# Optimization experiments

Measured on AMD Instinct MI355X. Metric: run time of the kernel, lower is better.

The kernel has to match this reference:

```python
import jax, jax.numpy as jnp
import numpy as np
import math

B, Q_LEN, D, H, KV = 8, 2048, 1024, 16, 256
HD = D // H

def setup_inputs() -> dict:
    key0 = jax.random.key(0)
    ks = jax.random.split(key0, 6)
    query = jax.random.normal(ks[0], (B, Q_LEN, D), dtype=jnp.float32)
    key = jax.random.normal(ks[1], (B, 1024), dtype=jnp.float32)
    value = jax.random.normal(ks[2], (B, 1024), dtype=jnp.float32)
    clip_score = jax.random.uniform(ks[3], (B, KV), dtype=jnp.float32)
    # k_linear / v_linear weights (embed_dim, 1024), no bias
    k_weight = jax.random.normal(ks[4], (D, 1024), dtype=jnp.float32) * 0.02
    v_weight = jax.random.normal(ks[5], (D, 1024), dtype=jnp.float32) * 0.02
    # scale_linear: Linear(512, 1), weight const 0.05, bias const 7.5 (per nn.init.constant_)
    scale_w = jnp.full((2 * KV,), 0.05, dtype=jnp.float32)
    scale_b = jnp.array(7.5, dtype=jnp.float32)
    return {"query": query, "key": key, "value": value, "clip_score": clip_score,
            "k_weight": k_weight, "v_weight": v_weight, "scale_w": scale_w, "scale_b": scale_b}

def reference(query, key, value, clip_score, k_weight, v_weight, scale_w, scale_b):
    act_scale = 1.0
    b, qlen, d = query.shape
    # key/value are (B,1024): expand to (B,KV,1024) as in torch branch
    key_e = jnp.broadcast_to(key[:, None, :], (b, KV, key.shape[-1]))
    val_e = jnp.broadcast_to(value[:, None, :], (b, KV, value.shape[-1]))
    K = jnp.einsum('bkc,dc->bkd', key_e, k_weight)   # (B,KV,D)
    V = jnp.einsum('bkc,dc->bkd', val_e, v_weight)   # (B,KV,D)
    Qh = query.reshape(b, qlen, H, HD).transpose(0, 2, 1, 3)  # (B,H,Q,HD)
    Kh = K.reshape(b, KV, H, HD).transpose(0, 2, 1, 3)        # (B,H,KV,HD)
    Vh = V.reshape(b, KV, H, HD).transpose(0, 2, 1, 3)        # (B,H,KV,HD)
    scores = jnp.einsum('bhqd,bhkd->bhqk', Qh, Kh) / math.sqrt(HD)  # (B,H,Q,KV)
    # scale_linear(cat([scores, clip], -1)) == scores@w1 + clip@w2 + b (avoid materializing concat)
    w1, w2 = scale_w[:KV], scale_w[KV:]
    lin = (jnp.einsum('bhqk,k->bhq', scores, w1)[..., None]
           + (clip_score @ w2)[:, None, None, None] + scale_b)   # (B,H,Q,1)
    clip_e = clip_score[:, None, None, :]                        # (B,1,1,KV)
    scores = scores + (lin * clip_e) * act_scale
    attn_weights = jax.nn.softmax(scores, axis=-1)
    out = jnp.einsum('bhqk,bhkd->bhqd', attn_weights, Vh)
    out = out.transpose(0, 2, 1, 3).reshape(b, qlen, d)
    return (out, attn_weights)
```

## Files before the change

### kernel.cpp

```cpp
#include <hip/hip_runtime.h>
#include <hip/hip_bf16.h>

#define B_    8
#define QLEN  2048
#define D_    1024
#define H_    16
#define KV_   256
#define HD_   64

typedef float fvec4 __attribute__((ext_vector_type(4)));

#define WS_KVEC 0
#define WS_VVEC 8192
#define WS_C2   16384
#define WS_SW1  16392
#define WS_L    16400

__device__ inline float wave_sum(float v) {
#pragma unroll
  for (int off = 32; off > 0; off >>= 1) v += __shfl_xor(v, off, 64);
  return v;
}
__device__ inline float wave_max(float v) {
#pragma unroll
  for (int off = 32; off > 0; off >>= 1) v = fmaxf(v, __shfl_xor(v, off, 64));
  return v;
}
__device__ inline float wave_min(float v) {
#pragma unroll
  for (int off = 32; off > 0; off >>= 1) v = fminf(v, __shfl_xor(v, off, 64));
  return v;
}
template <int N>
__device__ inline void multi_sum(float* v) {
#pragma unroll
  for (int off = 32; off > 0; off >>= 1) {
#pragma unroll
    for (int r = 0; r < N; ++r) v[r] += __shfl_xor(v[r], off, 64);
  }
}

__global__ __launch_bounds__(256) void prep_kernel(
    const float* __restrict__ key, const float* __restrict__ value,
    const float* __restrict__ kw, const float* __restrict__ vw,
    const float* __restrict__ clip, const float* __restrict__ scale_w,
    float* __restrict__ ws) {
  const int lane = threadIdx.x & 63;
  const int waveId = threadIdx.x >> 6;

  if (blockIdx.x == 1024) {
    if (waveId != 0) return;
    const float4* sw4 = reinterpret_cast<const float4*>(scale_w);
    float4 a = sw4[lane];
    float s = wave_sum(a.x + a.y + a.z + a.w);
    if (lane == 0) ws[WS_SW1] = s;
    float4 w2 = sw4[64 + lane];
    for (int b = 0; b < B_; ++b) {
      const float4* c4 = reinterpret_cast<const float4*>(clip + b * KV_);
      float4 c = c4[lane];
      float p = c.x * w2.x + c.y * w2.y + c.z * w2.z + c.w * w2.w;
      p = wave_sum(p);
      if (lane == 0) ws[WS_C2 + b] = p;
    }
    return;
  }

  const int W = blockIdx.x * 4 + waveId;
  const int sel = W >> 11;
  const int rem = W & 2047;
  const int b = rem >> 8;
  const int g = rem & 255;
  const float* x = (sel ? value : key) + b * 1024;
  const float* Wt = sel ? vw : kw;
  const float4* x4 = reinterpret_cast<const float4*>(x);
  float4 xs[4];
#pragma unroll
  for (int i = 0; i < 4; ++i) xs[i] = x4[i * 64 + lane];
  float* outv = ws + (sel ? WS_VVEC : WS_KVEC) + b * 1024;
  float acc[4];
#pragma unroll
  for (int r = 0; r < 4; ++r) {
    const int d = g * 4 + r;
    const float4* w4 = reinterpret_cast<const float4*>(Wt + (size_t)d * 1024);
    acc[r] = 0.f;
#pragma unroll
    for (int i = 0; i < 4; ++i) {
      float4 w = w4[i * 64 + lane];
      acc[r] += xs[i].x * w.x + xs[i].y * w.y + xs[i].z * w.z + xs[i].w * w.w;
    }
  }
  multi_sum<4>(acc);
  if (lane < 4) outv[g * 4 + lane] = acc[lane];
}

__global__ __launch_bounds__(256) void qdot_kernel(
    const float* __restrict__ query, const float* __restrict__ scale_b,
    float* __restrict__ ws) {
  const int lane = threadIdx.x & 63;
  const int waveId = threadIdx.x >> 6;
  const int rowBase = blockIdx.x * 64 + waveId * 16;
  const int b = rowBase >> 15;
  const int h = (rowBase >> 11) & 15;
  const int q0 = rowBase & 2047;
  const int g = lane >> 4;
  const int c = lane & 15;

  const fvec4 kvv = reinterpret_cast<const fvec4*>(ws + WS_KVEC + b * 1024 + h * HD_)[c];
  const float sw1 = ws[WS_SW1];
  const float Lc = ws[WS_C2 + b] + scale_b[0];

  const float* qb = query + ((size_t)(b * QLEN + q0)) * D_ + h * HD_;
  float p[4];
#pragma unroll
  for (int j = 0; j < 4; ++j) {
    const fvec4 q4 = __builtin_nontemporal_load(
        reinterpret_cast<const fvec4*>(qb + (size_t)(j * 4 + g) * D_) + c);
    p[j] = q4.x * kvv.x + q4.y * kvv.y + q4.z * kvv.z + q4.w * kvv.w;
  }
#pragma unroll
  for (int off = 1; off <= 8; off <<= 1) {
#pragma unroll
    for (int j = 0; j < 4; ++j) p[j] += __shfl_xor(p[j], off, 64);
  }
  if (c < 4) {
    const float sp = (c == 0) ? p[0] : (c == 1) ? p[1] : (c == 2) ? p[2] : p[3];
    ws[WS_L + rowBase + c * 4 + g] = sw1 * (sp * 0.125f) + Lc;
  }
}

__global__ __launch_bounds__(256) void stream_kernel(
    const float* __restrict__ clip, const float* __restrict__ ws,
    float* __restrict__ attn, float* __restrict__ out) {
  const int lane = threadIdx.x & 63;
  const int gwave = (blockIdx.x * 256 + threadIdx.x) >> 6;
  const int row0 = gwave * 32;
  const int b = row0 >> 15;

  const fvec4 cl = reinterpret_cast<const fvec4*>(clip + b * KV_)[lane];
  const float cmax = wave_max(fmaxf(fmaxf(cl.x, cl.y), fmaxf(cl.z, cl.w)));
  const float cmin = wave_min(fminf(fminf(cl.x, cl.y), fminf(cl.z, cl.w)));
  const float* Lp = ws + WS_L + row0;

  fvec4* a4 = reinterpret_cast<fvec4*>(attn) + (size_t)row0 * 64 + lane;
#pragma unroll 4
  for (int i = 0; i < 32; ++i) {
    const float Ld = Lp[i];
    const float m = (Ld >= 0.f) ? Ld * cmax : Ld * cmin;
    fvec4 e;
    e.x = __expf(Ld * cl.x - m);
    e.y = __expf(Ld * cl.y - m);
    e.z = __expf(Ld * cl.z - m);
    e.w = __expf(Ld * cl.w - m);
    const float den = wave_sum(e.x + e.y + e.z + e.w);
    e *= (1.0f / den);
    __builtin_nontemporal_store(e, &a4[(size_t)i * 64]);
  }

  const fvec4* v4 = reinterpret_cast<const fvec4*>(ws + WS_VVEC);
  fvec4* o4 = reinterpret_cast<fvec4*>(out);
#pragma unroll
  for (int i = 0; i < 8; ++i) {
    const int j = (gwave * 8 + i) * 64 + lane;
    const int ob = j >> 19;
    const int d4 = j & 255;
    fvec4 v = v4[ob * 256 + d4];
    __builtin_nontemporal_store(v, &o4[j]);
  }
}

extern "C" void kernel_launch(void* const* d_in, const int* in_sizes, int n_in,
                              void* d_out, int out_size, void* d_ws, size_t ws_size,
                              hipStream_t stream) {
  const float* query   = (const float*)d_in[0];
  const float* key     = (const float*)d_in[1];
  const float* value   = (const float*)d_in[2];
  const float* clip    = (const float*)d_in[3];
  const float* kw      = (const float*)d_in[4];
  const float* vw      = (const float*)d_in[5];
  const float* scale_w = (const float*)d_in[6];
  const float* scale_b = (const float*)d_in[7];
  float* out  = (float*)d_out;
  float* attn = out + (size_t)B_ * QLEN * D_;
  float* ws   = (float*)d_ws;

  hipLaunchKernelGGL(prep_kernel, dim3(1025), dim3(256), 0, stream,
                     key, value, kw, vw, clip, scale_w, ws);
  hipLaunchKernelGGL(qdot_kernel, dim3(4096), dim3(256), 0, stream,
                     query, scale_b, ws);
  hipLaunchKernelGGL(stream_kernel, dim3(2048), dim3(256), 0, stream,
                     clip, ws, attn, out);
}
```

Measured before the change: 82.93 us.

## Reuse weight rows across batches in prep and move out-broadcast into qdot kernel

The prep kernel now loads each weight row once into registers and loops over all 8 batches, so it launches 129 blocks instead of 1025 and stops re-reading the weight matrices 8 times. The broadcast write of V into the output tensor moves from the attention-stream kernel into extra blocks of the qdot kernel. This lets the output writes overlap with the query reads, and the stream kernel writes only attention weights. The stream kernel also fetches its 32 row coefficients in a single vector load and takes each one with readlane, with the loop fully unrolled.

```diff
diff --git a/kernel.cpp b/kernel.cpp
--- a/kernel.cpp
+++ b/kernel.cpp
@@ -48,16 +48,16 @@
   const int lane = threadIdx.x & 63;
   const int waveId = threadIdx.x >> 6;
 
-  if (blockIdx.x == 1024) {
+  if (blockIdx.x == 128) {
     if (waveId != 0) return;
-    const float4* sw4 = reinterpret_cast<const float4*>(scale_w);
-    float4 a = sw4[lane];
+    const fvec4* sw4 = reinterpret_cast<const fvec4*>(scale_w);
+    fvec4 a = sw4[lane];
     float s = wave_sum(a.x + a.y + a.z + a.w);
     if (lane == 0) ws[WS_SW1] = s;
-    float4 w2 = sw4[64 + lane];
+    fvec4 w2 = sw4[64 + lane];
     for (int b = 0; b < B_; ++b) {
-      const float4* c4 = reinterpret_cast<const float4*>(clip + b * KV_);
-      float4 c = c4[lane];
+      const fvec4* c4 = reinterpret_cast<const fvec4*>(clip + b * KV_);
+      fvec4 c = c4[lane];
       float p = c.x * w2.x + c.y * w2.y + c.z * w2.z + c.w * w2.w;
       p = wave_sum(p);
       if (lane == 0) ws[WS_C2 + b] = p;
@@ -66,39 +66,66 @@
   }
 
   const int W = blockIdx.x * 4 + waveId;
-  const int sel = W >> 11;
-  const int rem = W & 2047;
-  const int b = rem >> 8;
-  const int g = rem & 255;
-  const float* x = (sel ? value : key) + b * 1024;
+  const int sel = W >> 8;
+  const int g = W & 255;
   const float* Wt = sel ? vw : kw;
-  const float4* x4 = reinterpret_cast<const float4*>(x);
-  float4 xs[4];
-#pragma unroll
-  for (int i = 0; i < 4; ++i) xs[i] = x4[i * 64 + lane];
-  float* outv = ws + (sel ? WS_VVEC : WS_KVEC) + b * 1024;
-  float acc[4];
+  const float* xsrc = sel ? value : key;
+  float* outv = ws + (sel ? WS_VVEC : WS_KVEC);
+
+  fvec4 wr[4][4];
 #pragma unroll
   for (int r = 0; r < 4; ++r) {
-    const int d = g * 4 + r;
-    const float4* w4 = reinterpret_cast<const float4*>(Wt + (size_t)d * 1024);
-    acc[r] = 0.f;
-#pragma unroll
-    for (int i = 0; i < 4; ++i) {
-      float4 w = w4[i * 64 + lane];
-      acc[r] += xs[i].x * w.x + xs[i].y * w.y + xs[i].z * w.z + xs[i].w * w.w;
-    }
-  }
-  multi_sum<4>(acc);
-  if (lane < 4) outv[g * 4 + lane] = acc[lane];
-}
-
-__global__ __launch_bounds__(256) void qdot_kernel(
+    const fvec4* w4 = reinterpret_cast<const fvec4*>(Wt + (size_t)(g * 4 + r) * 1024);
+#pragma unroll
+    for (int i = 0; i < 4; ++i) wr[r][i] = w4[i * 64 + lane];
+  }
+
+  for (int b = 0; b < B_; ++b) {
+    const fvec4* x4 = reinterpret_cast<const fvec4*>(xsrc + b * 1024);
+    fvec4 xs[4];
+#pragma unroll
+    for (int i = 0; i < 4; ++i) xs[i] = x4[i * 64 + lane];
+    float acc[4];
+#pragma unroll
+    for (int r = 0; r < 4; ++r) {
+      acc[r] = 0.f;
+#pragma unroll
+      for (int i = 0; i < 4; ++i) {
+        acc[r] += xs[i].x * wr[r][i].x + xs[i].y * wr[r][i].y +
+                  xs[i].z * wr[r][i].z + xs[i].w * wr[r][i].w;
+      }
+    }
+    multi_sum<4>(acc);
+    if (lane < 4) {
+      const float v = (lane == 0) ? acc[0] : (lane == 1) ? acc[1]
+                    : (lane == 2) ? acc[2] : acc[3];
+      outv[b * 1024 + g * 4 + lane] = v;
+    }
+  }
+}
+
+__global__ __launch_bounds__(256) void qdot_out_kernel(
     const float* __restrict__ query, const float* __restrict__ scale_b,
-    float* __restrict__ ws) {
+    float* __restrict__ ws, float* __restrict__ out) {
   const int lane = threadIdx.x & 63;
+
+  if (blockIdx.x < 1024) {
+    const fvec4* v4 = reinterpret_cast<const fvec4*>(ws + WS_VVEC);
+    fvec4* o4 = reinterpret_cast<fvec4*>(out);
+    const int idx = blockIdx.x * 256 + threadIdx.x;
+#pragma unroll
+    for (int i = 0; i < 16; ++i) {
+      const int j = idx + i * 262144;
+      const int ob = j >> 19;
+      const int d4 = j & 255;
+      fvec4 v = v4[ob * 256 + d4];
+      __builtin_nontemporal_store(v, &o4[j]);
+    }
+    return;
+  }
+
   const int waveId = threadIdx.x >> 6;
-  const int rowBase = blockIdx.x * 64 + waveId * 16;
+  const int rowBase = (blockIdx.x - 1024) * 64 + waveId * 16;
   const int b = rowBase >> 15;
   const int h = (rowBase >> 11) & 15;
   const int q0 = rowBase & 2047;
@@ -128,9 +155,9 @@
   }
 }
 
-__global__ __launch_bounds__(256) void stream_kernel(
+__global__ __launch_bounds__(256) void attn_stream_kernel(
     const float* __restrict__ clip, const float* __restrict__ ws,
-    float* __restrict__ attn, float* __restrict__ out) {
+    float* __restrict__ attn) {
   const int lane = threadIdx.x & 63;
   const int gwave = (blockIdx.x * 256 + threadIdx.x) >> 6;
   const int row0 = gwave * 32;
@@ -139,12 +166,13 @@
   const fvec4 cl = reinterpret_cast<const fvec4*>(clip + b * KV_)[lane];
   const float cmax = wave_max(fmaxf(fmaxf(cl.x, cl.y), fmaxf(cl.z, cl.w)));
   const float cmin = wave_min(fminf(fminf(cl.x, cl.y), fminf(cl.z, cl.w)));
-  const float* Lp = ws + WS_L + row0;
+
+  const float Lv = ws[WS_L + row0 + (lane & 31)];
 
   fvec4* a4 = reinterpret_cast<fvec4*>(attn) + (size_t)row0 * 64 + lane;
-#pragma unroll 4
+#pragma unroll
   for (int i = 0; i < 32; ++i) {
-    const float Ld = Lp[i];
+    const float Ld = __builtin_amdgcn_readlane(Lv, i);
     const float m = (Ld >= 0.f) ? Ld * cmax : Ld * cmin;
     fvec4 e;
     e.x = __expf(Ld * cl.x - m);
@@ -154,17 +182,6 @@
     const float den = wave_sum(e.x + e.y + e.z + e.w);
     e *= (1.0f / den);
     __builtin_nontemporal_store(e, &a4[(size_t)i * 64]);
-  }
-
-  const fvec4* v4 = reinterpret_cast<const fvec4*>(ws + WS_VVEC);
-  fvec4* o4 = reinterpret_cast<fvec4*>(out);
-#pragma unroll
-  for (int i = 0; i < 8; ++i) {
-    const int j = (gwave * 8 + i) * 64 + lane;
-    const int ob = j >> 19;
-    const int d4 = j & 255;
-    fvec4 v = v4[ob * 256 + d4];
-    __builtin_nontemporal_store(v, &o4[j]);
   }
 }
 
@@ -183,10 +200,10 @@
   float* attn = out + (size_t)B_ * QLEN * D_;
   float* ws   = (float*)d_ws;
 
-  hipLaunchKernelGGL(prep_kernel, dim3(1025), dim3(256), 0, stream,
+  hipLaunchKernelGGL(prep_kernel, dim3(129), dim3(256), 0, stream,
                      key, value, kw, vw, clip, scale_w, ws);
-  hipLaunchKernelGGL(qdot_kernel, dim3(4096), dim3(256), 0, stream,
-                     query, scale_b, ws);
-  hipLaunchKernelGGL(stream_kernel, dim3(2048), dim3(256), 0, stream,
-                     clip, ws, attn, out);
-}
+  hipLaunchKernelGGL(qdot_out_kernel, dim3(5120), dim3(256), 0, stream,
+                     query, scale_b, ws, out);
+  hipLaunchKernelGGL(attn_stream_kernel, dim3(2048), dim3(256), 0, stream,
+                     clip, ws, attn);
+}
```

Measured after the change: 92.87 us. 1.12x slower.

## Fuse query-dot and softmax streaming kernels; load each weight row once in prep

Applied to the files above, without the earlier changes.

Merges the qdot and stream kernels into one. Each wave computes its 32 rows' scale logits in registers and broadcasts them with readlane, so the logit array no longer goes through the workspace and one launch is dropped. The prep kernel is restructured so each wave loads one weight row once and reuses it across all 8 batches, instead of rereading the weight matrix once per batch. This cuts weight traffic about eightfold and halves the prep grid, at the cost of more registers and fully unrolled loops in the fused kernel.

```diff
diff --git a/kernel.cpp b/kernel.cpp
--- a/kernel.cpp
+++ b/kernel.cpp
@@ -14,7 +14,6 @@
 #define WS_VVEC 8192
 #define WS_C2   16384
 #define WS_SW1  16392
-#define WS_L    16400
 
 __device__ inline float wave_sum(float v) {
 #pragma unroll
@@ -48,16 +47,16 @@
   const int lane = threadIdx.x & 63;
   const int waveId = threadIdx.x >> 6;
 
-  if (blockIdx.x == 1024) {
+  if (blockIdx.x == 512) {
     if (waveId != 0) return;
-    const float4* sw4 = reinterpret_cast<const float4*>(scale_w);
-    float4 a = sw4[lane];
+    const fvec4* sw4 = reinterpret_cast<const fvec4*>(scale_w);
+    fvec4 a = sw4[lane];
     float s = wave_sum(a.x + a.y + a.z + a.w);
     if (lane == 0) ws[WS_SW1] = s;
-    float4 w2 = sw4[64 + lane];
+    fvec4 w2 = sw4[64 + lane];
     for (int b = 0; b < B_; ++b) {
-      const float4* c4 = reinterpret_cast<const float4*>(clip + b * KV_);
-      float4 c = c4[lane];
+      const fvec4* c4 = reinterpret_cast<const fvec4*>(clip + b * KV_);
+      fvec4 c = c4[lane];
       float p = c.x * w2.x + c.y * w2.y + c.z * w2.z + c.w * w2.w;
       p = wave_sum(p);
       if (lane == 0) ws[WS_C2 + b] = p;
@@ -66,53 +65,72 @@
   }
 
   const int W = blockIdx.x * 4 + waveId;
-  const int sel = W >> 11;
-  const int rem = W & 2047;
-  const int b = rem >> 8;
-  const int g = rem & 255;
-  const float* x = (sel ? value : key) + b * 1024;
+  const int sel = W >> 10;
+  const int d = W & 1023;
   const float* Wt = sel ? vw : kw;
-  const float4* x4 = reinterpret_cast<const float4*>(x);
-  float4 xs[4];
+  const float* xsrc = sel ? value : key;
+  float* outv = ws + (sel ? WS_VVEC : WS_KVEC);
+
+  const fvec4* w4 = reinterpret_cast<const fvec4*>(Wt + (size_t)d * 1024);
+  fvec4 wr[4];
 #pragma unroll
-  for (int i = 0; i < 4; ++i) xs[i] = x4[i * 64 + lane];
-  float* outv = ws + (sel ? WS_VVEC : WS_KVEC) + b * 1024;
-  float acc[4];
+  for (int i = 0; i < 4; ++i) wr[i] = w4[i * 64 + lane];
+
 #pragma unroll
-  for (int r = 0; r < 4; ++r) {
-    const int d = g * 4 + r;
-    const float4* w4 = reinterpret_cast<const float4*>(Wt + (size_t)d * 1024);
-    acc[r] = 0.f;
+  for (int b0 = 0; b0 < B_; b0 += 2) {
+    const fvec4* xa = reinterpret_cast<const fvec4*>(xsrc + b0 * 1024);
+    const fvec4* xb = reinterpret_cast<const fvec4*>(xsrc + (b0 + 1) * 1024);
+    float acc[2] = {0.f, 0.f};
 #pragma unroll
     for (int i = 0; i < 4; ++i) {
-      float4 w = w4[i * 64 + lane];
-      acc[r] += xs[i].x * w.x + xs[i].y * w.y + xs[i].z * w.z + xs[i].w * w.w;
+      fvec4 x0 = xa[i * 64 + lane];
+      fvec4 x1 = xb[i * 64 + lane];
+      acc[0] += x0.x * wr[i].x + x0.y * wr[i].y + x0.z * wr[i].z + x0.w * wr[i].w;
+      acc[1] += x1.x * wr[i].x + x1.y * wr[i].y + x1.z * wr[i].z + x1.w * wr[i].w;
+    }
+    multi_sum<2>(acc);
+    if (lane == 0) {
+      outv[b0 * 1024 + d] = acc[0];
+      outv[(b0 + 1) * 1024 + d] = acc[1];
     }
   }
-  multi_sum<4>(acc);
-  if (lane < 4) outv[g * 4 + lane] = acc[lane];
 }
 
-__global__ __launch_bounds__(256) void qdot_kernel(
-    const float* __restrict__ query, const float* __restrict__ scale_b,
-    float* __restrict__ ws) {
+__global__ __launch_bounds__(256) void fused_kernel(
+    const float* __restrict__ query, const float* __restrict__ clip,
+    const float* __restrict__ scale_b, const float* __restrict__ ws,
+    float* __restrict__ attn, float* __restrict__ out) {
   const int lane = threadIdx.x & 63;
-  const int waveId = threadIdx.x >> 6;
-  const int rowBase = blockIdx.x * 64 + waveId * 16;
-  const int b = rowBase >> 15;
-  const int h = (rowBase >> 11) & 15;
-  const int q0 = rowBase & 2047;
+  const int gwave = (blockIdx.x * 256 + threadIdx.x) >> 6;
+  const int row0 = gwave * 32;
+  const int b = row0 >> 15;
+  const int h = (row0 >> 11) & 15;
+  const int q0 = row0 & 2047;
   const int g = lane >> 4;
   const int c = lane & 15;
 
-  const fvec4 kvv = reinterpret_cast<const fvec4*>(ws + WS_KVEC + b * 1024 + h * HD_)[c];
+  {
+    const fvec4* v4 = reinterpret_cast<const fvec4*>(ws + WS_VVEC);
+    fvec4* o4 = reinterpret_cast<fvec4*>(out);
+#pragma unroll
+    for (int i = 0; i < 8; ++i) {
+      const int j = (gwave * 8 + i) * 64 + lane;
+      const int ob = j >> 19;
+      const int d4 = j & 255;
+      fvec4 v = v4[ob * 256 + d4];
+      __builtin_nontemporal_store(v, &o4[j]);
+    }
+  }
+
+  const fvec4 kvv =
+      reinterpret_cast<const fvec4*>(ws + WS_KVEC + b * 1024 + h * HD_)[c];
   const float sw1 = ws[WS_SW1];
   const float Lc = ws[WS_C2 + b] + scale_b[0];
+  const float* qb = query + ((size_t)(b * QLEN + q0)) * D_ + h * HD_;
 
-  const float* qb = query + ((size_t)(b * QLEN + q0)) * D_ + h * HD_;
-  float p[4];
+  float p[8];
 #pragma unroll
-  for (int j = 0; j < 4; ++j) {
+  for (int j = 0; j < 8; ++j) {
     const fvec4 q4 = __builtin_nontemporal_load(
         reinterpret_cast<const fvec4*>(qb + (size_t)(j * 4 + g) * D_) + c);
     p[j] = q4.x * kvv.x + q4.y * kvv.y + q4.z * kvv.z + q4.w * kvv.w;
@@ -120,31 +138,19 @@
 #pragma unroll
   for (int off = 1; off <= 8; off <<= 1) {
 #pragma unroll
-    for (int j = 0; j < 4; ++j) p[j] += __shfl_xor(p[j], off, 64);
+    for (int j = 0; j < 8; ++j) p[j] += __shfl_xor(p[j], off, 64);
   }
-  if (c < 4) {
-    const float sp = (c == 0) ? p[0] : (c == 1) ? p[1] : (c == 2) ? p[2] : p[3];
-    ws[WS_L + rowBase + c * 4 + g] = sw1 * (sp * 0.125f) + Lc;
-  }
-}
-
-__global__ __launch_bounds__(256) void stream_kernel(
-    const float* __restrict__ clip, const float* __restrict__ ws,
-    float* __restrict__ attn, float* __restrict__ out) {
-  const int lane = threadIdx.x & 63;
-  const int gwave = (blockIdx.x * 256 + threadIdx.x) >> 6;
-  const int row0 = gwave * 32;
-  const int b = row0 >> 15;
+#pragma unroll
+  for (int j = 0; j < 8; ++j) p[j] = sw1 * (p[j] * 0.125f) + Lc;
 
   const fvec4 cl = reinterpret_cast<const fvec4*>(clip + b * KV_)[lane];
   const float cmax = wave_max(fmaxf(fmaxf(cl.x, cl.y), fmaxf(cl.z, cl.w)));
   const float cmin = wave_min(fminf(fminf(cl.x, cl.y), fminf(cl.z, cl.w)));
-  const float* Lp = ws + WS_L + row0;
 
   fvec4* a4 = reinterpret_cast<fvec4*>(attn) + (size_t)row0 * 64 + lane;
-#pragma unroll 4
+#pragma unroll
   for (int i = 0; i < 32; ++i) {
-    const float Ld = Lp[i];
+    const float Ld = __builtin_amdgcn_readlane(p[i >> 2], (i & 3) << 4);
     const float m = (Ld >= 0.f) ? Ld * cmax : Ld * cmin;
     fvec4 e;
     e.x = __expf(Ld * cl.x - m);
@@ -154,17 +160,6 @@
     const float den = wave_sum(e.x + e.y + e.z + e.w);
     e *= (1.0f / den);
     __builtin_nontemporal_store(e, &a4[(size_t)i * 64]);
-  }
-
-  const fvec4* v4 = reinterpret_cast<const fvec4*>(ws + WS_VVEC);
-  fvec4* o4 = reinterpret_cast<fvec4*>(out);
-#pragma unroll
-  for (int i = 0; i < 8; ++i) {
-    const int j = (gwave * 8 + i) * 64 + lane;
-    const int ob = j >> 19;
-    const int d4 = j & 255;
-    fvec4 v = v4[ob * 256 + d4];
-    __builtin_nontemporal_store(v, &o4[j]);
   }
 }
 
@@ -183,10 +178,8 @@
   float* attn = out + (size_t)B_ * QLEN * D_;
   float* ws   = (float*)d_ws;
 
-  hipLaunchKernelGGL(prep_kernel, dim3(1025), dim3(256), 0, stream,
+  hipLaunchKernelGGL(prep_kernel, dim3(513), dim3(256), 0, stream,
                      key, value, kw, vw, clip, scale_w, ws);
-  hipLaunchKernelGGL(qdot_kernel, dim3(4096), dim3(256), 0, stream,
-                     query, scale_b, ws);
-  hipLaunchKernelGGL(stream_kernel, dim3(2048), dim3(256), 0, stream,
-                     clip, ws, attn, out);
+  hipLaunchKernelGGL(fused_kernel, dim3(2048), dim3(256), 0, stream,
+                     query, clip, scale_b, ws, attn, out);
 }
```

After: 87.43 us. 1.05x slower.
